# Performance work log

Hardware: AMD Instinct MI355X
Metric: run time of the kernel (lower is better)

The kernel has to match this reference:

```python
import jax, jax.numpy as jnp
import numpy as np

B, S, D, H = 2, 2048, 1024, 16
DH = D // H  # 64


def setup_inputs() -> dict:
    key = jax.random.key(0)
    ks = jax.random.split(key, 7)
    scale = 0.02
    return {
        "q": jax.random.normal(ks[0], (B, S, D), dtype=jnp.float32),
        "k": jax.random.normal(ks[1], (B, S, D), dtype=jnp.float32),
        "v": jax.random.normal(ks[2], (B, S, D), dtype=jnp.float32),
        "Wq": jax.random.normal(ks[3], (D, D), dtype=jnp.float32) * scale,
        "Wk": jax.random.normal(ks[4], (D, D), dtype=jnp.float32) * scale,
        "Wv": jax.random.normal(ks[5], (D, D), dtype=jnp.float32) * scale,
        "Wo": jax.random.normal(ks[6], (D, D), dtype=jnp.float32) * scale,
    }


def _split_heads(x):
    # [B, S, D] -> [B, H, S, DH]
    b, s, d = x.shape
    return x.reshape(b, s, H, DH).transpose(0, 2, 1, 3)


def reference(q, k, v, Wq, Wk, Wv, Wo):
    # Linear projections (torch Linear: x @ W.T, bias=False)
    qh = _split_heads(q @ Wq.T)  # [B, H, S, DH]
    kh = _split_heads(k @ Wk.T)
    vh = _split_heads(v @ Wv.T)
    # Scaled dot-product attention (manual, materializes scores as original)
    scores = jnp.einsum("bhqd,bhkd->bhqk", qh, kh) / jnp.sqrt(
        jnp.asarray(DH, dtype=qh.dtype)
    )  # [B, H, S, S]
    attn = jax.nn.softmax(scores, axis=-1)
    out = jnp.einsum("bhqk,bhkd->bhqd", attn, vh)  # [B, H, S, DH]
    # Concat heads: [B, H, S, DH] -> [B, S, D]
    out = out.transpose(0, 2, 1, 3).reshape(q.shape[0], q.shape[1], D)
    return out @ Wo.T
```

## Files before the change

kernel.cpp:

```cpp
#include <hip/hip_runtime.h>
#include <hip/hip_bf16.h>
#include <math.h>

namespace {
constexpr int Hn  = 16;
constexpr int DH  = 64;
constexpr int S   = 2048;
constexpr int D   = 1024;
constexpr int B   = 2;
constexpr int N   = B * S;
}

typedef __attribute__((ext_vector_type(8))) short bf16x8;
typedef __attribute__((ext_vector_type(4))) float f32x4;

#if defined(__has_builtin)
#if __has_builtin(__builtin_amdgcn_exp2f)
#define HAVE_EXP2_BUILTIN 1
#endif
#endif

static __device__ __forceinline__ float exp2_fast(float x) {
#ifdef HAVE_EXP2_BUILTIN
    return __builtin_amdgcn_exp2f(x);
#else
    float r;
    asm("v_exp_f32 %0, %1" : "=v"(r) : "v"(x));
    return r;
#endif
}

static __device__ __forceinline__ ushort bf16rd(float x) {
    unsigned u = __builtin_bit_cast(unsigned, x);
    return (ushort)((u + 0x8000u) >> 16);
}
static __device__ __forceinline__ float bfu2f(ushort h) {
    unsigned u = (unsigned)h << 16;
    return __builtin_bit_cast(float, u);
}
static __device__ __forceinline__ void split1(float a, ushort& h, ushort& l) {
    h = bf16rd(a);
    l = bf16rd(a - bfu2f(h));
}

static __device__ __forceinline__ void gload16(const ushort* g, ushort* l) {
    __builtin_amdgcn_global_load_lds((const unsigned int*)g, (unsigned int*)l, 16, 0, 0);
}

__global__ __launch_bounds__(256) void split_all(
    const float4* __restrict__ q, const float4* __restrict__ k, const float4* __restrict__ v,
    const float4* __restrict__ wq, const float4* __restrict__ wk,
    const float4* __restrict__ wv, const float4* __restrict__ wo,
    ushort4* __restrict__ qh, ushort4* __restrict__ kh, ushort4* __restrict__ vh,
    ushort4* __restrict__ wqh, ushort4* __restrict__ wkh, ushort4* __restrict__ wvh,
    ushort4* __restrict__ woh, ushort4* __restrict__ wol,
    int n4a, int n4w) {
    const int total = 3 * n4a + 4 * n4w;
    const int stride = gridDim.x * 256;
    for (int i = blockIdx.x * 256 + threadIdx.x; i < total; i += stride) {
        if (i < 3 * n4a) {
            const int which = i / n4a;
            const int j = i - which * n4a;
            const float4 val = (which == 0 ? q : which == 1 ? k : v)[j];
            ushort4* ph = which == 0 ? qh : which == 1 ? kh : vh;
            ph[j] = make_ushort4(bf16rd(val.x), bf16rd(val.y), bf16rd(val.z), bf16rd(val.w));
        } else {
            const int t = i - 3 * n4a;
            const int which = t / n4w;
            const int j = t - which * n4w;
            const float4 val = (which == 0 ? wq : which == 1 ? wk : which == 2 ? wv : wo)[j];
            if (which == 3) {
                ushort4 hh, ll;
                split1(val.x, hh.x, ll.x);
                split1(val.y, hh.y, ll.y);
                split1(val.z, hh.z, ll.z);
                split1(val.w, hh.w, ll.w);
                woh[j] = hh;
                wol[j] = ll;
            } else {
                ushort4* ph = which == 0 ? wqh : which == 1 ? wkh : wvh;
                ph[j] = make_ushort4(bf16rd(val.x), bf16rd(val.y), bf16rd(val.z), bf16rd(val.w));
            }
        }
    }
}

__global__ __launch_bounds__(256) void gemm_qkv(
    const ushort* __restrict__ qbf, const ushort* __restrict__ kbf,
    const ushort* __restrict__ vbf,
    const ushort* __restrict__ Wqh, const ushort* __restrict__ Wkh,
    const ushort* __restrict__ Wvh,
    ushort* __restrict__ Qbh, ushort* __restrict__ Kbh,
    ushort* __restrict__ Vtb, float qscale) {
    constexpr int BK = 64;
    constexpr int K = D;
    __shared__ __align__(16) ushort sA[128 * BK];
    __shared__ __align__(16) ushort sB[128 * BK];

    const int tid = threadIdx.x;
    const int which = blockIdx.y >> 3;
    const int m0 = blockIdx.x * 128;
    const int n0 = (blockIdx.y & 7) * 128;

    const ushort* A = which == 0 ? qbf : which == 1 ? kbf : vbf;
    const ushort* W = which == 0 ? Wqh : which == 1 ? Wkh : Wvh;

    const int l  = tid & 63;
    const int w  = tid >> 6;
    const int wm = w >> 1, wn = w & 1;
    const int lm = l & 15, g = l >> 4;

    const int srow = l >> 3;
    const int schunk = (l & 7) ^ srow;
    const ushort* gA = A + (size_t)(m0 + w * 32 + srow) * K + schunk * 8;
    const ushort* gB = W + (size_t)(n0 + w * 32 + srow) * K + schunk * 8;
    ushort* lA = &sA[(w * 32) * BK];
    ushort* lB = &sB[(w * 32) * BK];

    const f32x4 fzero = {0.f, 0.f, 0.f, 0.f};
    f32x4 acc[4][4];
#pragma unroll
    for (int mi = 0; mi < 4; ++mi)
#pragma unroll
        for (int ni = 0; ni < 4; ++ni) acc[mi][ni] = fzero;

    const int rsw = lm & 7;

    for (int s = 0; s < K / BK; ++s) {
        const int k0 = s * BK;
        if (s) __syncthreads();
#pragma unroll
        for (int j = 0; j < 4; ++j) {
            gload16(gA + (size_t)(j * 8) * K + k0, lA + (j * 8) * BK);
            gload16(gB + (size_t)(j * 8) * K + k0, lB + (j * 8) * BK);
        }
        __syncthreads();

#pragma unroll
        for (int kk = 0; kk < 2; ++kk) {
            bf16x8 ah[4], bh[4];
#pragma unroll
            for (int mi = 0; mi < 4; ++mi)
                ah[mi] = *(const bf16x8*)&sA[(wm * 64 + mi * 16 + lm) * BK + (((kk * 4 + g) ^ rsw) * 8)];
#pragma unroll
            for (int ni = 0; ni < 4; ++ni)
                bh[ni] = *(const bf16x8*)&sB[(wn * 64 + ni * 16 + lm) * BK + (((kk * 4 + g) ^ rsw) * 8)];
            __builtin_amdgcn_s_setprio(1);
#pragma unroll
            for (int mi = 0; mi < 4; ++mi)
#pragma unroll
                for (int ni = 0; ni < 4; ++ni)
                    acc[mi][ni] = __builtin_amdgcn_mfma_f32_16x16x32_bf16(
                        ah[mi], bh[ni], acc[mi][ni], 0, 0, 0);
            __builtin_amdgcn_s_setprio(0);
        }
    }

#pragma unroll
    for (int mi = 0; mi < 4; ++mi)
#pragma unroll
        for (int ni = 0; ni < 4; ++ni) {
            const int col = n0 + wn * 64 + ni * 16 + lm;
            const int rbase = m0 + wm * 64 + mi * 16 + g * 4;
            const int hh = col >> 6, dh = col & (DH - 1);
            if (which == 0) {
#pragma unroll
                for (int r = 0; r < 4; ++r) {
                    const int row = rbase + r;
                    const int bb = row >> 11, ss = row & (S - 1);
                    const size_t idx = (((size_t)(bb * Hn + hh)) * S + ss) * DH + dh;
                    Qbh[idx] = bf16rd(acc[mi][ni][r] * qscale);
                }
            } else if (which == 1) {
#pragma unroll
                for (int r = 0; r < 4; ++r) {
                    const int row = rbase + r;
                    const int bb = row >> 11, ss = row & (S - 1);
                    const size_t idx = (((size_t)(bb * Hn + hh)) * S + ss) * DH + dh;
                    Kbh[idx] = bf16rd(acc[mi][ni][r]);
                }
            } else {
                const int bb = rbase >> 11, ss = rbase & (S - 1);
                const int ssp = (ss & ~31) | (((ss >> 2) & 3) << 3) | (((ss >> 4) & 1) << 2);
                ushort4 pk;
                pk.x = bf16rd(acc[mi][ni][0]);
                pk.y = bf16rd(acc[mi][ni][1]);
                pk.z = bf16rd(acc[mi][ni][2]);
                pk.w = bf16rd(acc[mi][ni][3]);
                const size_t idx = (((size_t)(bb * Hn + hh)) * DH + dh) * S + ssp;
                *(ushort4*)&Vtb[idx] = pk;
            }
        }
}

__global__ __launch_bounds__(256) void gemm_out(const ushort* __restrict__ Ah,
                                                const ushort* __restrict__ Al,
                                                const ushort* __restrict__ Wh,
                                                const ushort* __restrict__ Wl,
                                                float* __restrict__ C) {
    constexpr int BK = 32;
    constexpr int LDT = 40;
    constexpr int K = D, O = D;
    __shared__ __align__(16) ushort sAh[2][128 * LDT];
    __shared__ __align__(16) ushort sAl[2][128 * LDT];
    __shared__ __align__(16) ushort sBh[2][64 * LDT];
    __shared__ __align__(16) ushort sBl[2][64 * LDT];

    const int tid = threadIdx.x;
    const int m0 = blockIdx.x * 128;
    const int n0 = blockIdx.y * 64;

    const int l   = tid & 63;
    const int wid = tid >> 6;
    const int wm  = wid >> 1;
    const int wn  = wid & 1;
    const int lm  = l & 15;
    const int g   = l >> 4;
    const int lk  = g * 8;

    const int arow0 = tid >> 2;
    const int aslot = (tid & 3) * 8;
    const ushort* gAh0 = Ah + (size_t)(m0 + arow0) * K + aslot;
    const ushort* gAh1 = gAh0 + (size_t)64 * K;
    const ushort* gAl0 = Al + (size_t)(m0 + arow0) * K + aslot;
    const ushort* gAl1 = gAl0 + (size_t)64 * K;
    const ushort* gBh  = Wh + (size_t)(n0 + arow0) * K + aslot;
    const ushort* gBl  = Wl + (size_t)(n0 + arow0) * K + aslot;

    const f32x4 fzero = {0.f, 0.f, 0.f, 0.f};
    f32x4 acc[4][2];
#pragma unroll
    for (int mi = 0; mi < 4; ++mi)
#pragma unroll
        for (int ni = 0; ni < 2; ++ni) acc[mi][ni] = fzero;

    uint4 rA0 = *(const uint4*)gAh0, rA1 = *(const uint4*)gAh1;
    uint4 rA2 = *(const uint4*)gAl0, rA3 = *(const uint4*)gAl1;
    uint4 rB0 = *(const uint4*)gBh,  rB1 = *(const uint4*)gBl;

    *(uint4*)&sAh[0][arow0 * LDT + aslot]        = rA0;
    *(uint4*)&sAh[0][(arow0 + 64) * LDT + aslot] = rA1;
    *(uint4*)&sAl[0][arow0 * LDT + aslot]        = rA2;
    *(uint4*)&sAl[0][(arow0 + 64) * LDT + aslot] = rA3;
    *(uint4*)&sBh[0][arow0 * LDT + aslot]        = rB0;
    *(uint4*)&sBl[0][arow0 * LDT + aslot]        = rB1;
    rA0 = *(const uint4*)(gAh0 + BK); rA1 = *(const uint4*)(gAh1 + BK);
    rA2 = *(const uint4*)(gAl0 + BK); rA3 = *(const uint4*)(gAl1 + BK);
    rB0 = *(const uint4*)(gBh + BK);  rB1 = *(const uint4*)(gBl + BK);
    __syncthreads();

    constexpr int NS = K / BK;
    int cur = 0;
    for (int s = 0; s < NS; ++s) {
        bf16x8 ah[4], al[4], bh[2], bl[2];
#pragma unroll
        for (int mi = 0; mi < 4; ++mi) {
            const int row = wm * 64 + mi * 16 + lm;
            ah[mi] = *(const bf16x8*)&sAh[cur][row * LDT + lk];
            al[mi] = *(const bf16x8*)&sAl[cur][row * LDT + lk];
        }
#pragma unroll
        for (int ni = 0; ni < 2; ++ni) {
            const int rowb = wn * 32 + ni * 16 + lm;
            bh[ni] = *(const bf16x8*)&sBh[cur][rowb * LDT + lk];
            bl[ni] = *(const bf16x8*)&sBl[cur][rowb * LDT + lk];
        }
        __builtin_amdgcn_s_setprio(1);
#pragma unroll
        for (int mi = 0; mi < 4; ++mi)
#pragma unroll
            for (int ni = 0; ni < 2; ++ni) {
                acc[mi][ni] = __builtin_amdgcn_mfma_f32_16x16x32_bf16(
                    al[mi], bh[ni], acc[mi][ni], 0, 0, 0);
                acc[mi][ni] = __builtin_amdgcn_mfma_f32_16x16x32_bf16(
                    ah[mi], bl[ni], acc[mi][ni], 0, 0, 0);
                acc[mi][ni] = __builtin_amdgcn_mfma_f32_16x16x32_bf16(
                    ah[mi], bh[ni], acc[mi][ni], 0, 0, 0);
            }
        __builtin_amdgcn_s_setprio(0);

        if (s < NS - 1) {
            const int nx = cur ^ 1;
            *(uint4*)&sAh[nx][arow0 * LDT + aslot]        = rA0;
            *(uint4*)&sAh[nx][(arow0 + 64) * LDT + aslot] = rA1;
            *(uint4*)&sAl[nx][arow0 * LDT + aslot]        = rA2;
            *(uint4*)&sAl[nx][(arow0 + 64) * LDT + aslot] = rA3;
            *(uint4*)&sBh[nx][arow0 * LDT + aslot]        = rB0;
            *(uint4*)&sBl[nx][arow0 * LDT + aslot]        = rB1;
            if (s < NS - 2) {
                const int kn = (s + 2) * BK;
                rA0 = *(const uint4*)(gAh0 + kn); rA1 = *(const uint4*)(gAh1 + kn);
                rA2 = *(const uint4*)(gAl0 + kn); rA3 = *(const uint4*)(gAl1 + kn);
                rB0 = *(const uint4*)(gBh + kn);  rB1 = *(const uint4*)(gBl + kn);
            }
            __syncthreads();
            cur = nx;
        }
    }

#pragma unroll
    for (int mi = 0; mi < 4; ++mi)
#pragma unroll
        for (int ni = 0; ni < 2; ++ni) {
            const int col = n0 + wn * 32 + ni * 16 + lm;
            const int rbase = m0 + wm * 64 + mi * 16 + g * 4;
#pragma unroll
            for (int r = 0; r < 4; ++r)
                C[(size_t)(rbase + r) * O + col] = acc[mi][ni][r];
        }
}

__global__ __launch_bounds__(512) void attn_mfma(const ushort* __restrict__ Qbh,
                                                 const ushort* __restrict__ Kbh,
                                                 const ushort* __restrict__ Vt,
                                                 ushort* __restrict__ AOh,
                                                 ushort* __restrict__ AOl) {
    constexpr int LDT = 72;
    __shared__ __align__(16) ushort pool[4 * 64 * LDT];

    const int tid = threadIdx.x;
    const int l = tid & 63, w = tid >> 6;
    const int wq = w & 3, grp = w >> 2;
    const int g = l >> 4, l15 = l & 15;
    const int bh = blockIdx.x;
    const int q0 = blockIdx.y * 128;
    const size_t bhb = (size_t)bh * S * DH;

    ushort* Ksg = pool + grp * (64 * LDT);
    ushort* Vsg = pool + (2 + grp) * (64 * LDT);

    bf16x8 qh_[2][2];
#pragma unroll
    for (int qb = 0; qb < 2; ++qb)
#pragma unroll
        for (int kk = 0; kk < 2; ++kk) {
            const size_t idx = bhb + (size_t)(q0 + wq * 32 + qb * 16 + l15) * DH + kk * 32 + g * 8;
            qh_[qb][kk] = *(const bf16x8*)(Qbh + idx);
        }

    const int t8 = tid & 255;
    const int r_st = t8 >> 2;
    const int c0 = (t8 & 3) * 16;
    const ushort* gKh = Kbh + bhb + (size_t)r_st * DH + c0;
    const ushort* gVt = Vt + (size_t)bh * DH * S + (size_t)r_st * S + c0;

    const f32x4 fzero = {0.f, 0.f, 0.f, 0.f};
    f32x4 o_acc[2][4];
    f32x4 l_acc[2];
#pragma unroll
    for (int qb = 0; qb < 2; ++qb) {
        l_acc[qb] = fzero;
#pragma unroll
        for (int f = 0; f < 4; ++f) o_acc[qb][f] = fzero;
    }

    bf16x8 ones;
#pragma unroll
    for (int i = 0; i < 8; ++i) ones[i] = (short)0x3F80;

    uint4 pk0, pk1, pv0, pv1;
    {
        const size_t ok = (size_t)grp * 64 * DH, ov = (size_t)grp * 64;
        pk0 = *(const uint4*)(gKh + ok); pk1 = *(const uint4*)(gKh + ok + 8);
        pv0 = *(const uint4*)(gVt + ov); pv1 = *(const uint4*)(gVt + ov + 8);
        *(uint4*)&Ksg[r_st * LDT + c0]     = pk0;
        *(uint4*)&Ksg[r_st * LDT + c0 + 8] = pk1;
        *(uint4*)&Vsg[r_st * LDT + c0]     = pv0;
        *(uint4*)&Vsg[r_st * LDT + c0 + 8] = pv1;
        const size_t ok2 = (size_t)(2 + grp) * 64 * DH, ov2 = (size_t)(2 + grp) * 64;
        pk0 = *(const uint4*)(gKh + ok2); pk1 = *(const uint4*)(gKh + ok2 + 8);
        pv0 = *(const uint4*)(gVt + ov2); pv1 = *(const uint4*)(gVt + ov2 + 8);
    }
    __syncthreads();

    constexpr int NSI = S / 128;
    for (int t = 0; t < NSI; ++t) {
        f32x4 sc[2][4];
#pragma unroll
        for (int qb = 0; qb < 2; ++qb)
#pragma unroll
            for (int f = 0; f < 4; ++f) sc[qb][f] = fzero;
#pragma unroll
        for (int kk = 0; kk < 2; ++kk) {
            bf16x8 kh[4];
#pragma unroll
            for (int f = 0; f < 4; ++f)
                kh[f] = *(const bf16x8*)&Ksg[(f * 16 + l15) * LDT + kk * 32 + g * 8];
            __builtin_amdgcn_s_setprio(1);
#pragma unroll
            for (int f = 0; f < 4; ++f)
#pragma unroll
                for (int qb = 0; qb < 2; ++qb)
                    sc[qb][f] = __builtin_amdgcn_mfma_f32_16x16x32_bf16(
                        kh[f], qh_[qb][kk], sc[qb][f], 0, 0, 0);
            __builtin_amdgcn_s_setprio(0);
        }

        unsigned up[2][2][4];
#pragma unroll
        for (int qb = 0; qb < 2; ++qb)
#pragma unroll
            for (int f = 0; f < 4; ++f) {
                const int kk = f >> 1, a = f & 1;
                const unsigned e0 = __builtin_bit_cast(unsigned, exp2_fast(sc[qb][f][0]));
                const unsigned e1 = __builtin_bit_cast(unsigned, exp2_fast(sc[qb][f][1]));
                const unsigned e2 = __builtin_bit_cast(unsigned, exp2_fast(sc[qb][f][2]));
                const unsigned e3 = __builtin_bit_cast(unsigned, exp2_fast(sc[qb][f][3]));
                up[qb][kk][a * 2 + 0] = (e0 >> 16) | (e1 & 0xFFFF0000u);
                up[qb][kk][a * 2 + 1] = (e2 >> 16) | (e3 & 0xFFFF0000u);
            }

#pragma unroll
        for (int kk = 0; kk < 2; ++kk) {
            const bf16x8 pa0 = __builtin_bit_cast(bf16x8,
                make_uint4(up[0][kk][0], up[0][kk][1], up[0][kk][2], up[0][kk][3]));
            const bf16x8 pa1 = __builtin_bit_cast(bf16x8,
                make_uint4(up[1][kk][0], up[1][kk][1], up[1][kk][2], up[1][kk][3]));
            __builtin_amdgcn_s_setprio(1);
            l_acc[0] = __builtin_amdgcn_mfma_f32_16x16x32_bf16(pa0, ones, l_acc[0], 0, 0, 0);
            l_acc[1] = __builtin_amdgcn_mfma_f32_16x16x32_bf16(pa1, ones, l_acc[1], 0, 0, 0);
#pragma unroll
            for (int f = 0; f < 4; ++f) {
                const bf16x8 vt = *(const bf16x8*)&Vsg[(f * 16 + l15) * LDT + kk * 32 + g * 8];
                o_acc[0][f] = __builtin_amdgcn_mfma_f32_16x16x32_bf16(pa0, vt, o_acc[0][f], 0, 0, 0);
                o_acc[1][f] = __builtin_amdgcn_mfma_f32_16x16x32_bf16(pa1, vt, o_acc[1][f], 0, 0, 0);
            }
            __builtin_amdgcn_s_setprio(0);
        }

        __syncthreads();
        if (t < NSI - 1) {
            *(uint4*)&Ksg[r_st * LDT + c0]     = pk0;
            *(uint4*)&Ksg[r_st * LDT + c0 + 8] = pk1;
            *(uint4*)&Vsg[r_st * LDT + c0]     = pv0;
            *(uint4*)&Vsg[r_st * LDT + c0 + 8] = pv1;
            if (t < NSI - 2) {
                const size_t ok = (size_t)(2 * (t + 2) + grp) * 64 * DH;
                const size_t ov = (size_t)(2 * (t + 2) + grp) * 64;
                pk0 = *(const uint4*)(gKh + ok); pk1 = *(const uint4*)(gKh + ok + 8);
                pv0 = *(const uint4*)(gVt + ov); pv1 = *(const uint4*)(gVt + ov + 8);
            }
            __syncthreads();
        }
    }

    float* comb  = (float*)pool;
    float* lcomb = comb + 4 * 32 * 64;
    __syncthreads();
    if (grp == 1) {
#pragma unroll
        for (int qb = 0; qb < 2; ++qb)
#pragma unroll
            for (int r = 0; r < 4; ++r) {
                const int row = qb * 16 + g * 4 + r;
#pragma unroll
                for (int f = 0; f < 4; ++f)
                    comb[wq * 2048 + row * 64 + f * 16 + l15] = o_acc[qb][f][r];
                if (l15 == 0) lcomb[wq * 32 + row] = l_acc[qb][r];
            }
    }
    __syncthreads();
    if (grp == 0) {
        const int bb = bh >> 4, hh = bh & 15;
#pragma unroll
        for (int qb = 0; qb < 2; ++qb)
#pragma unroll
            for (int r = 0; r < 4; ++r) {
                const int row = qb * 16 + g * 4 + r;
                const float lsum = l_acc[qb][r] + lcomb[wq * 32 + row];
                const float inv = 1.f / lsum;
                const int srow = q0 + wq * 32 + row;
#pragma unroll
                for (int f = 0; f < 4; ++f) {
                    const float val =
                        (o_acc[qb][f][r] + comb[wq * 2048 + row * 64 + f * 16 + l15]) * inv;
                    const size_t idx = ((size_t)(bb * S + srow)) * D + hh * DH + f * 16 + l15;
                    ushort hi, lo;
                    split1(val, hi, lo);
                    AOh[idx] = hi;
                    AOl[idx] = lo;
                }
            }
    }
}

extern "C" void kernel_launch(void* const* d_in, const int* in_sizes, int n_in,
                              void* d_out, int out_size, void* d_ws, size_t ws_size,
                              hipStream_t stream) {
    (void)in_sizes; (void)n_in; (void)out_size; (void)ws_size;
    const float* q  = (const float*)d_in[0];
    const float* k  = (const float*)d_in[1];
    const float* v  = (const float*)d_in[2];
    const float* Wq = (const float*)d_in[3];
    const float* Wk = (const float*)d_in[4];
    const float* Wv = (const float*)d_in[5];
    const float* Wo = (const float*)d_in[6];
    float* out = (float*)d_out;

    uint8_t* w8 = (uint8_t*)d_ws;
    constexpr size_t MB = 1u << 20;
    ushort* Wqh = (ushort*)(w8 + 0 * MB);
    ushort* Wkh = (ushort*)(w8 + 2 * MB);
    ushort* Wvh = (ushort*)(w8 + 4 * MB);
    ushort* Woh = (ushort*)(w8 + 6 * MB);
    ushort* Wol = (ushort*)(w8 + 8 * MB);
    ushort* qbf = (ushort*)(w8 + 16 * MB);
    ushort* kbf = (ushort*)(w8 + 24 * MB);
    ushort* vbf = (ushort*)(w8 + 32 * MB);
    ushort* Qbh = (ushort*)(w8 + 40 * MB);
    ushort* Kbh = (ushort*)(w8 + 48 * MB);
    ushort* Vtb = (ushort*)(w8 + 56 * MB);
    ushort* AOh = (ushort*)(w8 + 64 * MB);
    ushort* AOl = (ushort*)(w8 + 72 * MB);

    const int n4_act = (N * D) / 4;
    const int n4_w   = (D * D) / 4;
    const dim3 blk(256);

    split_all<<<2048, blk, 0, stream>>>(
        (const float4*)q, (const float4*)k, (const float4*)v,
        (const float4*)Wq, (const float4*)Wk, (const float4*)Wv, (const float4*)Wo,
        (ushort4*)qbf, (ushort4*)kbf, (ushort4*)vbf,
        (ushort4*)Wqh, (ushort4*)Wkh, (ushort4*)Wvh,
        (ushort4*)Woh, (ushort4*)Wol,
        n4_act, n4_w);

    const float qscale = 0.125f * 1.4426950408889634f;
    gemm_qkv<<<dim3(N / 128, 24), blk, 0, stream>>>(
        qbf, kbf, vbf, Wqh, Wkh, Wvh, Qbh, Kbh, Vtb, qscale);

    attn_mfma<<<dim3(B * Hn, S / 128), dim3(512), 0, stream>>>(
        Qbh, Kbh, Vtb, AOh, AOl);

    gemm_out<<<dim3(N / 128, D / 64), blk, 0, stream>>>(AOh, AOl, Woh, Wol, out);
}
```

Measured before the change: 138.5 us.

## Use direct global-to-LDS swizzled loads in output GEMM and halve attention blocks

The output-projection GEMM drops its register-staged, double-buffered padded LDS tiles. It now uses gload16 direct global-to-LDS copies into a single XOR-swizzled buffer with BK=64, and does two MFMA k-substeps per stage. This is meant to cut register pressure and LDS-store instructions, but it gives up overlap between loads and compute. The attention kernel moves from 512 to 256 threads per block with 64 query rows per block, which doubles the grid for better occupancy and load balance. Its K/V staging changes to four 16-byte loads per thread, and one redundant barrier before the combine step is removed.

```diff
diff --git a/kernel.cpp b/kernel.cpp
--- a/kernel.cpp
+++ b/kernel.cpp
@@ -198,34 +198,32 @@
                                                 const ushort* __restrict__ Wh,
                                                 const ushort* __restrict__ Wl,
                                                 float* __restrict__ C) {
-    constexpr int BK = 32;
-    constexpr int LDT = 40;
+    constexpr int BK = 64;
     constexpr int K = D, O = D;
-    __shared__ __align__(16) ushort sAh[2][128 * LDT];
-    __shared__ __align__(16) ushort sAl[2][128 * LDT];
-    __shared__ __align__(16) ushort sBh[2][64 * LDT];
-    __shared__ __align__(16) ushort sBl[2][64 * LDT];
+    __shared__ __align__(16) ushort sAh[128 * BK];
+    __shared__ __align__(16) ushort sAl[128 * BK];
+    __shared__ __align__(16) ushort sBh[64 * BK];
+    __shared__ __align__(16) ushort sBl[64 * BK];
 
     const int tid = threadIdx.x;
     const int m0 = blockIdx.x * 128;
     const int n0 = blockIdx.y * 64;
 
-    const int l   = tid & 63;
-    const int wid = tid >> 6;
-    const int wm  = wid >> 1;
-    const int wn  = wid & 1;
-    const int lm  = l & 15;
-    const int g   = l >> 4;
-    const int lk  = g * 8;
-
-    const int arow0 = tid >> 2;
-    const int aslot = (tid & 3) * 8;
-    const ushort* gAh0 = Ah + (size_t)(m0 + arow0) * K + aslot;
-    const ushort* gAh1 = gAh0 + (size_t)64 * K;
-    const ushort* gAl0 = Al + (size_t)(m0 + arow0) * K + aslot;
-    const ushort* gAl1 = gAl0 + (size_t)64 * K;
-    const ushort* gBh  = Wh + (size_t)(n0 + arow0) * K + aslot;
-    const ushort* gBl  = Wl + (size_t)(n0 + arow0) * K + aslot;
+    const int l  = tid & 63;
+    const int w  = tid >> 6;
+    const int wm = w >> 1, wn = w & 1;
+    const int lm = l & 15, g = l >> 4;
+
+    const int srow = l >> 3;
+    const int schunk = (l & 7) ^ srow;
+    const ushort* gAh = Ah + (size_t)(m0 + w * 32 + srow) * K + schunk * 8;
+    const ushort* gAl = Al + (size_t)(m0 + w * 32 + srow) * K + schunk * 8;
+    const ushort* gBh = Wh + (size_t)(n0 + w * 16 + srow) * K + schunk * 8;
+    const ushort* gBl = Wl + (size_t)(n0 + w * 16 + srow) * K + schunk * 8;
+    ushort* lAh = &sAh[(w * 32) * BK];
+    ushort* lAl = &sAl[(w * 32) * BK];
+    ushort* lBh = &sBh[(w * 16) * BK];
+    ushort* lBl = &sBl[(w * 16) * BK];
 
     const f32x4 fzero = {0.f, 0.f, 0.f, 0.f};
     f32x4 acc[4][2];
@@ -234,67 +232,52 @@
 #pragma unroll
         for (int ni = 0; ni < 2; ++ni) acc[mi][ni] = fzero;
 
-    uint4 rA0 = *(const uint4*)gAh0, rA1 = *(const uint4*)gAh1;
-    uint4 rA2 = *(const uint4*)gAl0, rA3 = *(const uint4*)gAl1;
-    uint4 rB0 = *(const uint4*)gBh,  rB1 = *(const uint4*)gBl;
-
-    *(uint4*)&sAh[0][arow0 * LDT + aslot]        = rA0;
-    *(uint4*)&sAh[0][(arow0 + 64) * LDT + aslot] = rA1;
-    *(uint4*)&sAl[0][arow0 * LDT + aslot]        = rA2;
-    *(uint4*)&sAl[0][(arow0 + 64) * LDT + aslot] = rA3;
-    *(uint4*)&sBh[0][arow0 * LDT + aslot]        = rB0;
-    *(uint4*)&sBl[0][arow0 * LDT + aslot]        = rB1;
-    rA0 = *(const uint4*)(gAh0 + BK); rA1 = *(const uint4*)(gAh1 + BK);
-    rA2 = *(const uint4*)(gAl0 + BK); rA3 = *(const uint4*)(gAl1 + BK);
-    rB0 = *(const uint4*)(gBh + BK);  rB1 = *(const uint4*)(gBl + BK);
-    __syncthreads();
-
-    constexpr int NS = K / BK;
-    int cur = 0;
-    for (int s = 0; s < NS; ++s) {
-        bf16x8 ah[4], al[4], bh[2], bl[2];
-#pragma unroll
-        for (int mi = 0; mi < 4; ++mi) {
-            const int row = wm * 64 + mi * 16 + lm;
-            ah[mi] = *(const bf16x8*)&sAh[cur][row * LDT + lk];
-            al[mi] = *(const bf16x8*)&sAl[cur][row * LDT + lk];
-        }
-#pragma unroll
-        for (int ni = 0; ni < 2; ++ni) {
-            const int rowb = wn * 32 + ni * 16 + lm;
-            bh[ni] = *(const bf16x8*)&sBh[cur][rowb * LDT + lk];
-            bl[ni] = *(const bf16x8*)&sBl[cur][rowb * LDT + lk];
-        }
-        __builtin_amdgcn_s_setprio(1);
-#pragma unroll
-        for (int mi = 0; mi < 4; ++mi)
+    const int rsw = lm & 7;
+
+    for (int s = 0; s < K / BK; ++s) {
+        const int k0 = s * BK;
+        if (s) __syncthreads();
+#pragma unroll
+        for (int j = 0; j < 4; ++j) {
+            gload16(gAh + (size_t)(j * 8) * K + k0, lAh + (j * 8) * BK);
+            gload16(gAl + (size_t)(j * 8) * K + k0, lAl + (j * 8) * BK);
+        }
+#pragma unroll
+        for (int j = 0; j < 2; ++j) {
+            gload16(gBh + (size_t)(j * 8) * K + k0, lBh + (j * 8) * BK);
+            gload16(gBl + (size_t)(j * 8) * K + k0, lBl + (j * 8) * BK);
+        }
+        __syncthreads();
+
+#pragma unroll
+        for (int kk = 0; kk < 2; ++kk) {
+            const int rc = ((kk * 4 + g) ^ rsw) * 8;
+            bf16x8 ah[4], al[4], bh[2], bl[2];
+#pragma unroll
+            for (int mi = 0; mi < 4; ++mi) {
+                const int row = wm * 64 + mi * 16 + lm;
+                ah[mi] = *(const bf16x8*)&sAh[row * BK + rc];
+                al[mi] = *(const bf16x8*)&sAl[row * BK + rc];
+            }
 #pragma unroll
             for (int ni = 0; ni < 2; ++ni) {
-                acc[mi][ni] = __builtin_amdgcn_mfma_f32_16x16x32_bf16(
-                    al[mi], bh[ni], acc[mi][ni], 0, 0, 0);
-                acc[mi][ni] = __builtin_amdgcn_mfma_f32_16x16x32_bf16(
-                    ah[mi], bl[ni], acc[mi][ni], 0, 0, 0);
-                acc[mi][ni] = __builtin_amdgcn_mfma_f32_16x16x32_bf16(
-                    ah[mi], bh[ni], acc[mi][ni], 0, 0, 0);
-            }
-        __builtin_amdgcn_s_setprio(0);
-
-        if (s < NS - 1) {
-            const int nx = cur ^ 1;
-            *(uint4*)&sAh[nx][arow0 * LDT + aslot]        = rA0;
-            *(uint4*)&sAh[nx][(arow0 + 64) * LDT + aslot] = rA1;
-            *(uint4*)&sAl[nx][arow0 * LDT + aslot]        = rA2;
-            *(uint4*)&sAl[nx][(arow0 + 64) * LDT + aslot] = rA3;
-            *(uint4*)&sBh[nx][arow0 * LDT + aslot]        = rB0;
-            *(uint4*)&sBl[nx][arow0 * LDT + aslot]        = rB1;
-            if (s < NS - 2) {
-                const int kn = (s + 2) * BK;
-                rA0 = *(const uint4*)(gAh0 + kn); rA1 = *(const uint4*)(gAh1 + kn);
-                rA2 = *(const uint4*)(gAl0 + kn); rA3 = *(const uint4*)(gAl1 + kn);
-                rB0 = *(const uint4*)(gBh + kn);  rB1 = *(const uint4*)(gBl + kn);
-            }
-            __syncthreads();
-            cur = nx;
+                const int rowb = wn * 32 + ni * 16 + lm;
+                bh[ni] = *(const bf16x8*)&sBh[rowb * BK + rc];
+                bl[ni] = *(const bf16x8*)&sBl[rowb * BK + rc];
+            }
+            __builtin_amdgcn_s_setprio(1);
+#pragma unroll
+            for (int mi = 0; mi < 4; ++mi)
+#pragma unroll
+                for (int ni = 0; ni < 2; ++ni) {
+                    acc[mi][ni] = __builtin_amdgcn_mfma_f32_16x16x32_bf16(
+                        al[mi], bh[ni], acc[mi][ni], 0, 0, 0);
+                    acc[mi][ni] = __builtin_amdgcn_mfma_f32_16x16x32_bf16(
+                        ah[mi], bl[ni], acc[mi][ni], 0, 0, 0);
+                    acc[mi][ni] = __builtin_amdgcn_mfma_f32_16x16x32_bf16(
+                        ah[mi], bh[ni], acc[mi][ni], 0, 0, 0);
+                }
+            __builtin_amdgcn_s_setprio(0);
         }
     }
 
@@ -310,7 +293,7 @@
         }
 }
 
-__global__ __launch_bounds__(512) void attn_mfma(const ushort* __restrict__ Qbh,
+__global__ __launch_bounds__(256) void attn_mfma(const ushort* __restrict__ Qbh,
                                                  const ushort* __restrict__ Kbh,
                                                  const ushort* __restrict__ Vt,
                                                  ushort* __restrict__ AOh,
@@ -320,10 +303,10 @@
 
     const int tid = threadIdx.x;
     const int l = tid & 63, w = tid >> 6;
-    const int wq = w & 3, grp = w >> 2;
+    const int wq = w & 1, grp = w >> 1;
     const int g = l >> 4, l15 = l & 15;
     const int bh = blockIdx.x;
-    const int q0 = blockIdx.y * 128;
+    const int q0 = blockIdx.y * 64;
     const size_t bhb = (size_t)bh * S * DH;
 
     ushort* Ksg = pool + grp * (64 * LDT);
@@ -338,9 +321,9 @@
             qh_[qb][kk] = *(const bf16x8*)(Qbh + idx);
         }
 
-    const int t8 = tid & 255;
-    const int r_st = t8 >> 2;
-    const int c0 = (t8 & 3) * 16;
+    const int t7 = tid & 127;
+    const int r_st = t7 >> 1;
+    const int c0 = (t7 & 1) * 32;
     const ushort* gKh = Kbh + bhb + (size_t)r_st * DH + c0;
     const ushort* gVt = Vt + (size_t)bh * DH * S + (size_t)r_st * S + c0;
 
@@ -358,18 +341,25 @@
 #pragma unroll
     for (int i = 0; i < 8; ++i) ones[i] = (short)0x3F80;
 
-    uint4 pk0, pk1, pv0, pv1;
+    uint4 pk[4], pv[4];
     {
         const size_t ok = (size_t)grp * 64 * DH, ov = (size_t)grp * 64;
-        pk0 = *(const uint4*)(gKh + ok); pk1 = *(const uint4*)(gKh + ok + 8);
-        pv0 = *(const uint4*)(gVt + ov); pv1 = *(const uint4*)(gVt + ov + 8);
-        *(uint4*)&Ksg[r_st * LDT + c0]     = pk0;
-        *(uint4*)&Ksg[r_st * LDT + c0 + 8] = pk1;
-        *(uint4*)&Vsg[r_st * LDT + c0]     = pv0;
-        *(uint4*)&Vsg[r_st * LDT + c0 + 8] = pv1;
+#pragma unroll
+        for (int j = 0; j < 4; ++j) {
+            pk[j] = *(const uint4*)(gKh + ok + j * 8);
+            pv[j] = *(const uint4*)(gVt + ov + j * 8);
+        }
+#pragma unroll
+        for (int j = 0; j < 4; ++j) {
+            *(uint4*)&Ksg[r_st * LDT + c0 + j * 8] = pk[j];
+            *(uint4*)&Vsg[r_st * LDT + c0 + j * 8] = pv[j];
+        }
         const size_t ok2 = (size_t)(2 + grp) * 64 * DH, ov2 = (size_t)(2 + grp) * 64;
-        pk0 = *(const uint4*)(gKh + ok2); pk1 = *(const uint4*)(gKh + ok2 + 8);
-        pv0 = *(const uint4*)(gVt + ov2); pv1 = *(const uint4*)(gVt + ov2 + 8);
+#pragma unroll
+        for (int j = 0; j < 4; ++j) {
+            pk[j] = *(const uint4*)(gKh + ok2 + j * 8);
+            pv[j] = *(const uint4*)(gVt + ov2 + j * 8);
+        }
     }
     __syncthreads();
 
@@ -430,23 +420,26 @@
 
         __syncthreads();
         if (t < NSI - 1) {
-            *(uint4*)&Ksg[r_st * LDT + c0]     = pk0;
-            *(uint4*)&Ksg[r_st * LDT + c0 + 8] = pk1;
-            *(uint4*)&Vsg[r_st * LDT + c0]     = pv0;
-            *(uint4*)&Vsg[r_st * LDT + c0 + 8] = pv1;
+#pragma unroll
+            for (int j = 0; j < 4; ++j) {
+                *(uint4*)&Ksg[r_st * LDT + c0 + j * 8] = pk[j];
+                *(uint4*)&Vsg[r_st * LDT + c0 + j * 8] = pv[j];
+            }
             if (t < NSI - 2) {
                 const size_t ok = (size_t)(2 * (t + 2) + grp) * 64 * DH;
                 const size_t ov = (size_t)(2 * (t + 2) + grp) * 64;
-                pk0 = *(const uint4*)(gKh + ok); pk1 = *(const uint4*)(gKh + ok + 8);
-                pv0 = *(const uint4*)(gVt + ov); pv1 = *(const uint4*)(gVt + ov + 8);
+#pragma unroll
+                for (int j = 0; j < 4; ++j) {
+                    pk[j] = *(const uint4*)(gKh + ok + j * 8);
+                    pv[j] = *(const uint4*)(gVt + ov + j * 8);
+                }
             }
             __syncthreads();
         }
     }
 
     float* comb  = (float*)pool;
-    float* lcomb = comb + 4 * 32 * 64;
-    __syncthreads();
+    float* lcomb = comb + 2 * 32 * 64;
     if (grp == 1) {
 #pragma unroll
         for (int qb = 0; qb < 2; ++qb)
@@ -529,7 +522,7 @@
     gemm_qkv<<<dim3(N / 128, 24), blk, 0, stream>>>(
         qbf, kbf, vbf, Wqh, Wkh, Wvh, Qbh, Kbh, Vtb, qscale);
 
-    attn_mfma<<<dim3(B * Hn, S / 128), dim3(512), 0, stream>>>(
+    attn_mfma<<<dim3(B * Hn, S / 64), blk, 0, stream>>>(
         Qbh, Kbh, Vtb, AOh, AOl);
 
     gemm_out<<<dim3(N / 128, D / 64), blk, 0, stream>>>(AOh, AOl, Woh, Wol, out);
```

Result: slower. 238.6 us (+72.3%).
